# Performance work log

Measured on AMD Instinct MI355X. Metric: run time of the kernel, lower is better.

## Reference

```python
import jax, jax.numpy as jnp
import numpy as np

N, IN_DIM, LAT, NB = 4096, 3000, 64, 2
SINKHORN_ITERS = 3


def _bce_logits(x, y):
    # torch BCEWithLogitsLoss, mean reduction, numerically stable
    return jnp.mean(jnp.maximum(x, 0.0) - x * y + jnp.log1p(jnp.exp(-jnp.abs(x))))


def _forward(feature_set, adj_set, graph_neigh_set, label_CSL_set, dist_mat_set,
             enc_W, dec_W, Ms, disc_W, disc_b, perm_idx):
    nb = feature_set.shape[0]
    hs = []
    loss_sl = 0.0
    loss_feat = 0.0
    for k in range(nb):  # small fixed loop over slices
        x, adj, mask, lab = feature_set[k], adj_set[k], graph_neigh_set[k], label_CSL_set[k]
        h = adj @ (x @ enc_W[k])            # GCN encode: spmm(adj, x @ W)
        out = adj @ (h @ dec_W[k])          # GCN decode
        x_a = x[perm_idx[k]]                # permutation(x): row shuffle
        h_a = adj @ (x_a @ enc_W[k])
        hr, har = jax.nn.relu(h), jax.nn.relu(h_a)

        def readout(emb):
            vsum = mask @ emb
            ge = vsum / mask.sum(1, keepdims=True)
            nrm = jnp.linalg.norm(ge, axis=1, keepdims=True)
            return ge / jnp.maximum(nrm, 1e-12)   # F.normalize p=2

        g = jax.nn.sigmoid(readout(hr))
        g_a = jax.nn.sigmoid(readout(har))

        def disc(c, hp, hm):
            s1 = jnp.einsum('nd,de,ne->n', hp, disc_W, c) + disc_b[0]
            s2 = jnp.einsum('nd,de,ne->n', hm, disc_W, c) + disc_b[0]
            return jnp.stack([s1, s2], axis=1)  # [N,2]

        ret = disc(g, hr, har)
        ret_a = disc(g_a, har, hr)
        loss_sl = loss_sl + _bce_logits(ret, lab) + _bce_logits(ret_a, lab)
        loss_feat = loss_feat + jnp.mean((x - out) ** 2)
        hs.append(h)

    loss_align = 0.0; loss_align_fix = 0.0; loss_maintain = 0.0
    loss_marginal = 0.0; loss_sparsity = 0.0
    for k in range(1, nb):
        src, tgt = hs[k - 1], hs[k]
        M = Ms[k - 1]
        m1, m2 = src.shape[0], tgt.shape[0]
        C = (src @ M) @ (tgt @ M).T / jnp.sqrt(jnp.float32(M.shape[0]))
        P = jax.nn.softmax(C, axis=1) / m1
        # NonSquareSinkhornKnopp.fit: alternate row/col normalization to uniform marginals
        for _ in range(SINKHORN_ITERS):
            P = P / (m1 * P.sum(1, keepdims=True))
            P = P / (m2 * P.sum(0, keepdims=True))
        cxy = P / P.sum(1, keepdims=True)
        cyx = P.T / P.T.sum(1, keepdims=True)
        # cdist(src, tgt)
        d2 = jnp.sum(src ** 2, 1)[:, None] + jnp.sum(tgt ** 2, 1)[None, :] - 2.0 * (src @ tgt.T)
        cd = jnp.sqrt(jnp.maximum(d2, 1e-12))
        loss_align = loss_align + jnp.sum(P * cd)
        f0, f1 = feature_set[k - 1], feature_set[k]
        loss_align_fix = loss_align_fix + jnp.mean((f0 - cxy @ f1) ** 2) + jnp.mean((f1 - cyx @ f0) ** 2)
        D0, D1 = dist_mat_set[k - 1], dist_mat_set[k]
        diff1 = D0 - cxy @ (D1 @ cxy.T)
        diff2 = D1 - cyx @ (D0 @ cyx.T)
        loss_maintain = loss_maintain + jnp.linalg.norm(diff1) / m1 + jnp.linalg.norm(diff2) / m2
        # replicate torch F.kl_div(input, target) = mean(target*(log target - input))
        p = jnp.full((m2,), 1.0 / m2, jnp.float32)
        q = P.sum(0)
        kld_pq = jnp.mean(q * (jnp.log(q) - p))
        kld_pp = jnp.mean(p * (jnp.log(p) - p))
        loss_marginal = loss_marginal + (kld_pq - kld_pp) * m2
        loss_sparsity = loss_sparsity - jnp.sum(P * jnp.log(P + 1e-10))
    return jnp.stack([loss_sl, loss_feat, loss_align, loss_align_fix,
                      loss_maintain, loss_marginal, loss_sparsity])


def setup_inputs():
    key = jax.random.key(0)
    ks = jax.random.split(key, 12)
    feature_set = jax.random.normal(ks[0], (NB, N, IN_DIM), jnp.float32)
    A = jax.random.uniform(ks[1], (NB, N, N), jnp.float32)
    adj_set = A / A.sum(-1, keepdims=True)  # row-stochastic dense stand-in for normalized sparse adj
    mask = (jax.random.uniform(ks[2], (NB, N, N)) < 0.01).astype(jnp.float32)
    graph_neigh_set = mask + jnp.eye(N, dtype=jnp.float32)[None]  # nonzero row sums
    lab = jnp.concatenate([jnp.ones((N, 1)), jnp.zeros((N, 1))], axis=1).astype(jnp.float32)
    label_CSL_set = jnp.broadcast_to(lab, (NB, N, 2))
    D = jax.random.uniform(ks[3], (NB, N, N), jnp.float32)
    dist_mat_set = 0.5 * (D + jnp.swapaxes(D, 1, 2))
    perm_idx = jnp.stack([jax.random.permutation(ks[4 + i], N) for i in range(NB)]).astype(jnp.int32)
    s_enc = np.float32(np.sqrt(2.0 / (IN_DIM + LAT)))
    enc_W = jax.random.normal(ks[6], (NB, IN_DIM, LAT), jnp.float32) * s_enc
    dec_W = jax.random.normal(ks[7], (NB, LAT, IN_DIM), jnp.float32) * s_enc
    s_lat = np.float32(np.sqrt(1.0 / LAT))
    Ms = jax.random.normal(ks[8], (NB - 1, LAT, LAT), jnp.float32) * s_lat
    disc_W = jax.random.normal(ks[9], (LAT, LAT), jnp.float32) * s_lat
    disc_b = jnp.zeros((1,), jnp.float32)
    return dict(feature_set=feature_set, adj_set=adj_set, graph_neigh_set=graph_neigh_set,
                label_CSL_set=label_CSL_set, dist_mat_set=dist_mat_set, perm_idx=perm_idx,
                enc_W=enc_W, dec_W=dec_W, Ms=Ms, disc_W=disc_W, disc_b=disc_b)


def reference(feature_set, adj_set, graph_neigh_set, label_CSL_set, dist_mat_set,
              perm_idx, enc_W, dec_W, Ms, disc_W, disc_b):
    return _forward(feature_set, adj_set, graph_neigh_set, label_CSL_set, dist_mat_set,
                    enc_W, dec_W, Ms, disc_W, disc_b, perm_idx)
```

## Files before the change

kernel.cpp:

```cpp
#include <hip/hip_runtime.h>
#include <cmath>

constexpr int kN   = 4096;
constexpr int kIN  = 3000;
constexpr int kINp = 3072;
constexpr int kLAT = 64;

enum { SL = 0, FEAT, ALN, FXA, FXB, SM1, SM2, SPS, NSLOT };

typedef __bf16 bf16x8 __attribute__((ext_vector_type(8)));
typedef float f32x4 __attribute__((ext_vector_type(4)));
typedef unsigned short u16x8 __attribute__((ext_vector_type(8)));
typedef unsigned short u16x4 __attribute__((ext_vector_type(4)));

template<bool IS_MAX>
__device__ __forceinline__ float blk_red(float v) {
  __shared__ float buf[8];
  #pragma unroll
  for (int s = 32; s > 0; s >>= 1) {
    float o = __shfl_down(v, s, 64);
    v = IS_MAX ? fmaxf(v, o) : (v + o);
  }
  int lane = threadIdx.x & 63, wv = threadIdx.x >> 6, nw = blockDim.x >> 6;
  __syncthreads();
  if (lane == 0) buf[wv] = v;
  __syncthreads();
  float r = buf[0];
  for (int i = 1; i < nw; i++) r = IS_MAX ? fmaxf(r, buf[i]) : (r + buf[i]);
  return r;
}

__device__ __forceinline__ float wave_red_sum(float v) {
  #pragma unroll
  for (int s = 32; s > 0; s >>= 1) v += __shfl_down(v, s, 64);
  return v;
}

__device__ __forceinline__ unsigned short f2bf(float f) {
  unsigned u = __builtin_bit_cast(unsigned, f);
  u += 0x7fffu + ((u >> 16) & 1u);
  return (unsigned short)(u >> 16);
}
__device__ __forceinline__ float bf2f(unsigned short h) {
  return __builtin_bit_cast(float, (unsigned)h << 16);
}

__device__ __forceinline__ void gload16(const unsigned short* g, unsigned short* l) {
  __builtin_amdgcn_global_load_lds(
      (const __attribute__((address_space(1))) unsigned int*)g,
      (__attribute__((address_space(3))) unsigned int*)l, 16, 0, 0);
}

#define VMW(n) asm volatile("s_waitcnt vmcnt(" #n ")" ::: "memory")

__global__ __launch_bounds__(512, 2)
void g8_mfma_k(const unsigned short* __restrict__ A, const unsigned short* __restrict__ Bt,
               unsigned short* __restrict__ Cb, const float* __restrict__ rowdiv, int K)
{
  __shared__ unsigned short AB[65536];

  int orig = blockIdx.x;
  int x = orig & 7, tt = orig >> 3;
  int bx = tt >> 1, by = x * 2 + (tt & 1);
  const int row0 = by * 256, col0 = bx * 256;

  const int t = threadIdx.x, l = t & 63, wv = t >> 6;
  const int wr = wv >> 2, wc = wv & 3;
  const int lr = l & 15;
  const int sA = (l >> 4) ^ ((lr >> 1) & 3);

  f32x4 acc[8][4];
  #pragma unroll
  for (int i = 0; i < 8; i++)
    #pragma unroll
    for (int j = 0; j < 4; j++) acc[i][j] = (f32x4){0.f, 0.f, 0.f, 0.f};

  const int NT = K >> 6;
  const int NI = NT >> 1;

  const int srow  = l >> 2;
  const int sslot = (l & 3) ^ ((l >> 3) & 3);
  const unsigned short* Ap = A  + (size_t)(row0 + srow) * K + sslot * 8;
  const unsigned short* Bp = Bt + (size_t)(col0 + srow) * K + sslot * 8;

  auto STG = [&](int tile, int r) {
    if (tile >= NT) return;
    int buf = tile & 1, ks = r >> 1;
    const unsigned short* src = (r & 1) ? Bp : Ap;
    unsigned short* dst = AB + buf * 32768 + r * 8192;
    size_t koff = (size_t)tile * 64 + ks * 32;
    #pragma unroll
    for (int j = 0; j < 2; j++) {
      int c = wv * 2 + j;
      gload16(src + (size_t)c * 16 * K + koff, dst + c * 512);
    }
  };

  u16x8 af[8], bfv[2];

#define MFMA16(AV, BV, ACC) \
  ACC = __builtin_amdgcn_mfma_f32_16x16x32_bf16( \
      __builtin_bit_cast(bf16x8, AV), __builtin_bit_cast(bf16x8, BV), ACC, 0, 0, 0)

#define PH_A(WN, BUF, KS, STILE, SR)                                           \
  {                                                                            \
    if ((WN) == 8) VMW(8); else if ((WN) == 4) VMW(4);                         \
    else if ((WN) == 0) VMW(0);                                                \
    __builtin_amdgcn_s_barrier();                                              \
    {                                                                          \
      const unsigned short* ab = &AB[(BUF) * 32768 + (KS) * 16384];            \
      _Pragma("unroll")                                                        \
      for (int mi = 0; mi < 8; mi++)                                           \
        af[mi] = *(const u16x8*)&ab[(wr * 128 + mi * 16 + lr) * 32 + sA * 8];  \
      const unsigned short* bb = ab + 8192;                                    \
      bfv[0] = *(const u16x8*)&bb[(wc * 64 +  0 + lr) * 32 + sA * 8];          \
      bfv[1] = *(const u16x8*)&bb[(wc * 64 + 16 + lr) * 32 + sA * 8];          \
    }                                                                          \
    if ((STILE) >= 0) STG(STILE, SR);                                          \
    asm volatile("s_waitcnt lgkmcnt(0)" ::: "memory");                         \
    __builtin_amdgcn_sched_barrier(0);                                         \
    __builtin_amdgcn_s_setprio(1);                                             \
    _Pragma("unroll")                                                          \
    for (int mi = 0; mi < 8; mi++) {                                           \
      MFMA16(af[mi], bfv[0], acc[mi][0]);                                      \
      MFMA16(af[mi], bfv[1], acc[mi][1]);                                      \
    }                                                                          \
    __builtin_amdgcn_s_setprio(0);                                             \
    __builtin_amdgcn_s_barrier();                                              \
  }

#define PH_B(BUF, KS, STILE, SR)                                               \
  {                                                                            \
    __builtin_amdgcn_s_barrier();                                              \
    {                                                                          \
      const unsigned short* bb = &AB[(BUF) * 32768 + (KS) * 16384 + 8192];     \
      bfv[0] = *(const u16x8*)&bb[(wc * 64 + 32 + lr) * 32 + sA * 8];          \
      bfv[1] = *(const u16x8*)&bb[(wc * 64 + 48 + lr) * 32 + sA * 8];          \
    }                                                                          \
    if ((STILE) >= 0) STG(STILE, SR);                                          \
    asm volatile("s_waitcnt lgkmcnt(0)" ::: "memory");                         \
    __builtin_amdgcn_sched_barrier(0);                                         \
    __builtin_amdgcn_s_setprio(1);                                             \
    _Pragma("unroll")                                                          \
    for (int mi = 0; mi < 8; mi++) {                                           \
      MFMA16(af[mi], bfv[0], acc[mi][2]);                                      \
      MFMA16(af[mi], bfv[1], acc[mi][3]);                                      \
    }                                                                          \
    __builtin_amdgcn_s_setprio(0);                                             \
    __builtin_amdgcn_s_barrier();                                              \
  }

  STG(0, 0); STG(0, 1); STG(0, 2); STG(0, 3); STG(1, 0); STG(1, 1);

  for (int i = 0; i < NI - 1; ++i) {
    int T = 2 * i;
    PH_A(8, 0, 0, T + 1, 2);
    PH_B(   0, 0, T + 1, 3);
    PH_A(8, 0, 1, T + 2, 0);
    PH_B(   0, 1, T + 2, 1);
    PH_A(8, 1, 0, T + 2, 2);
    PH_B(   1, 0, T + 2, 3);
    PH_A(8, 1, 1, T + 3, 0);
    PH_B(   1, 1, T + 3, 1);
  }
  {
    int T = 2 * (NI - 1);
    PH_A(8, 0, 0, T + 1, 2);
    PH_B(   0, 0, T + 1, 3);
    PH_A(8, 0, 1, -1, 0);
    PH_B(   0, 1, -1, 0);
    PH_A(4, 1, 0, -1, 0);
    PH_B(   1, 0, -1, 0);
    PH_A(0, 1, 1, -1, 0);
    PH_B(   1, 1, -1, 0);
  }
#undef PH_A
#undef PH_B
#undef MFMA16

  const int lcol = l & 15, lrow = (l >> 4) << 2;
  #pragma unroll
  for (int mi = 0; mi < 8; mi++) {
    int rr = row0 + wr * 128 + mi * 16 + lrow;
    #pragma unroll
    for (int nn = 0; nn < 4; nn++) {
      int cc = col0 + wc * 64 + nn * 16 + lcol;
      #pragma unroll
      for (int r = 0; r < 4; r++) {
        float v = acc[mi][nn][r];
        if (rowdiv) v /= rowdiv[rr + r];
        Cb[(size_t)(rr + r) * 4096 + cc] = f2bf(v);
      }
    }
  }
}

template<int EPI, int XBF>
__global__ __launch_bounds__(256)
void bt_mfma_k(const unsigned short* __restrict__ A, const unsigned short* __restrict__ Bt,
               unsigned short* __restrict__ Cb, float* __restrict__ Cf,
               const void* __restrict__ Xv,
               const float* __restrict__ rowdiv, const float* __restrict__ coldiv,
               float* __restrict__ slot, int gx, int Nc, int K, int ldX, int sym)
{
  __shared__ unsigned short AB[3 * 8192];

  int orig = blockIdx.x;
  int bx, by;
  if (EPI == 2 && sym) {
    int x = orig & 7, i = orig >> 3;
    int u = x * 66 + i;
    float disc = 4225.f - 8.f * (float)u;
    by = (int)((65.f - sqrtf(fmaxf(disc, 0.f))) * 0.5f);
    while (by > 0 && 32 * by - by * (by - 1) / 2 > u) by--;
    while (32 * (by + 1) - (by + 1) * by / 2 <= u) by++;
    bx = by + (u - (32 * by - by * (by - 1) / 2));
  } else {
    int x = orig & 7, tt = orig >> 3;
    bx = tt >> 2;
    by = x * 4 + (tt & 3);
  }
  const int row0 = by * 128, col0 = bx * 128;

  const int t = threadIdx.x, l = t & 63, wv = t >> 6;
  const int wr = wv >> 1, wc = wv & 1;
  const int lr = l & 15, lkh = (l >> 4) << 3;

  f32x4 acc[4][4];
  #pragma unroll
  for (int i = 0; i < 4; i++)
    #pragma unroll
    for (int j = 0; j < 4; j++) acc[i][j] = (f32x4){0.f, 0.f, 0.f, 0.f};

  const int srow = l >> 2;
  const int sk   = (l & 3) << 3;
  const unsigned short* Ab = A  + (size_t)(row0 + srow) * K + sk;
  const unsigned short* Bb = Bt + (size_t)(col0 + srow) * K + sk;

  const int NT = K >> 5;

  auto STAGE = [&](int kt, int buf) {
    unsigned short* As = AB + buf * 8192;
    unsigned short* Bs = As + 4096;
    int k0 = kt << 5;
    #pragma unroll
    for (int h2 = 0; h2 < 2; h2++) {
      int c = wv * 2 + h2;
      gload16(Ab + (size_t)c * 16 * K + k0, As + c * 512);
      gload16(Bb + (size_t)c * 16 * K + k0, Bs + c * 512);
    }
  };

  STAGE(0, 0);
  if (NT > 1) STAGE(1, 1);
  if (NT > 2) STAGE(2, 2);
  int cur = 0;

  for (int kt = 0; kt < NT; ++kt) {
    int ahead = NT - 1 - kt;
    if (ahead >= 2)      { VMW(8); }
    else if (ahead == 1) { VMW(4); }
    else                 { VMW(0); }
    __builtin_amdgcn_sched_barrier(0);
    __builtin_amdgcn_s_barrier();

    const unsigned short* As = AB + cur * 8192;
    const unsigned short* Bs = As + 4096;
    u16x8 af[4], bfv[4];
    #pragma unroll
    for (int mi = 0; mi < 4; mi++)
      af[mi] = *(const u16x8*)&As[(wr * 64 + mi * 16 + lr) * 32 + lkh];
    #pragma unroll
    for (int ni = 0; ni < 4; ni++)
      bfv[ni] = *(const u16x8*)&Bs[(wc * 64 + ni * 16 + lr) * 32 + lkh];
    #pragma unroll
    for (int mi = 0; mi < 4; mi++)
      #pragma unroll
      for (int ni = 0; ni < 4; ni++)
        acc[mi][ni] = __builtin_amdgcn_mfma_f32_16x16x32_bf16(
            __builtin_bit_cast(bf16x8, af[mi]),
            __builtin_bit_cast(bf16x8, bfv[ni]), acc[mi][ni], 0, 0, 0);

    __builtin_amdgcn_s_barrier();
    if (kt + 3 < NT) STAGE(kt + 3, cur);
    cur = (cur == 2) ? 0 : cur + 1;
  }

  const int lcol = l & 15, lrow = (l >> 4) << 2;
  if (EPI == 1) {
    #pragma unroll
    for (int mi = 0; mi < 4; mi++) {
      int rr = row0 + wr * 64 + mi * 16 + lrow;
      #pragma unroll
      for (int ni = 0; ni < 4; ni++) {
        int cc = col0 + wc * 64 + ni * 16 + lcol;
        #pragma unroll
        for (int r = 0; r < 4; r++)
          Cf[(size_t)(rr + r) * 4096 + cc] = acc[mi][ni][r];
      }
    }
  } else if (EPI == 2) {
    const float* Xf = (const float*)Xv;
    const unsigned short* Xh = (const unsigned short*)Xv;
    float part = 0.f;
    #pragma unroll
    for (int mi = 0; mi < 4; mi++) {
      int rr = row0 + wr * 64 + mi * 16 + lrow;
      #pragma unroll
      for (int ni = 0; ni < 4; ni++) {
        int cc = col0 + wc * 64 + ni * 16 + lcol;
        if (cc < Nc) {
          float cd = coldiv ? coldiv[cc] : 1.f;
          #pragma unroll
          for (int r = 0; r < 4; r++) {
            float v = acc[mi][ni][r];
            if (rowdiv) v /= rowdiv[rr + r];
            v /= cd;
            size_t xi = (size_t)(rr + r) * ldX + cc;
            float xval = XBF ? bf2f(Xh[xi]) : Xf[xi];
            float d = xval - v;
            part = fmaf(d, d, part);
          }
        }
      }
    }
    part = blk_red<false>(part);
    if (t == 0) {
      float wgt = (sym && col0 > row0) ? 2.f : 1.f;
      atomicAdd(slot, part * wgt);
    }
  } else {
    const unsigned short* Ph = (const unsigned short*)Xv;
    float a = 0.f, sp = 0.f;
    #pragma unroll
    for (int mi = 0; mi < 4; mi++) {
      int rr = row0 + wr * 64 + mi * 16 + lrow;
      #pragma unroll
      for (int ni = 0; ni < 4; ni++) {
        int cc = col0 + wc * 64 + ni * 16 + lcol;
        #pragma unroll
        for (int r = 0; r < 4; r++) {
          float g = acc[mi][ni][r];
          float p = bf2f(Ph[(size_t)(rr + r) * ldX + cc]);
          float d2 = rowdiv[rr + r] + coldiv[cc] - 2.f * g;
          a = fmaf(p, sqrtf(fmaxf(d2, 1e-12f)), a);
          sp = fmaf(p, logf(p + 1e-10f), sp);
        }
      }
    }
    a = blk_red<false>(a);
    sp = blk_red<false>(sp);
    if (t == 0) { atomicAdd(&slot[ALN], a); atomicAdd(&slot[SPS], sp); }
  }
}

__global__ __launch_bounds__(256)
void ns_mfma_k(const unsigned short* __restrict__ A, const unsigned short* __restrict__ Bt,
               float* __restrict__ C, int Nc, int K, int KC, int ldC)
{
  __shared__ unsigned short AB[2 * 8192];
  int ks = blockIdx.x & 15, strip = blockIdx.x >> 4;
  const int row0 = strip * 128;
  const int kbase = ks * KC;

  const int t = threadIdx.x, l = t & 63, wv = t >> 6;
  const int wr = wv >> 1, wc = wv & 1;
  const int lr = l & 15, lkh = (l >> 4) << 3;

  f32x4 acc[4][4];
  #pragma unroll
  for (int i = 0; i < 4; i++)
    #pragma unroll
    for (int j = 0; j < 4; j++) acc[i][j] = (f32x4){0.f, 0.f, 0.f, 0.f};

  const int srow = l >> 2;
  const int sk   = (l & 3) << 3;
  const unsigned short* Ab = A  + (size_t)(row0 + srow) * K + kbase + sk;
  const unsigned short* Bb = Bt + (size_t)srow * K + kbase + sk;

  const int NT = KC >> 5;

  auto STAGE = [&](int kt, int buf) {
    unsigned short* As = AB + buf * 8192;
    unsigned short* Bs = As + 4096;
    int k0 = kt << 5;
    #pragma unroll
    for (int h2 = 0; h2 < 2; h2++) {
      int c = wv * 2 + h2;
      gload16(Ab + (size_t)c * 16 * K + k0, As + c * 512);
      gload16(Bb + (size_t)c * 16 * K + k0, Bs + c * 512);
    }
  };

  STAGE(0, 0);
  if (NT > 1) STAGE(1, 1);
  int cur = 0;

  for (int kt = 0; kt < NT; ++kt) {
    if (kt + 1 < NT) { VMW(4); }
    else             { VMW(0); }
    __builtin_amdgcn_sched_barrier(0);
    __builtin_amdgcn_s_barrier();

    const unsigned short* As = AB + cur * 8192;
    const unsigned short* Bs = As + 4096;
    u16x8 af[4], bfv[4];
    #pragma unroll
    for (int mi = 0; mi < 4; mi++)
      af[mi] = *(const u16x8*)&As[(wr * 64 + mi * 16 + lr) * 32 + lkh];
    #pragma unroll
    for (int ni = 0; ni < 4; ni++)
      bfv[ni] = *(const u16x8*)&Bs[(wc * 64 + ni * 16 + lr) * 32 + lkh];
    #pragma unroll
    for (int mi = 0; mi < 4; mi++)
      #pragma unroll
      for (int ni = 0; ni < 4; ni++)
        acc[mi][ni] = __builtin_amdgcn_mfma_f32_16x16x32_bf16(
            __builtin_bit_cast(bf16x8, af[mi]),
            __builtin_bit_cast(bf16x8, bfv[ni]), acc[mi][ni], 0, 0, 0);

    __builtin_amdgcn_s_barrier();
    if (kt + 2 < NT) STAGE(kt + 2, cur);
    cur ^= 1;
  }

  const int lcol = l & 15, lrow = (l >> 4) << 2;
  #pragma unroll
  for (int mi = 0; mi < 4; mi++) {
    int rr = row0 + wr * 64 + mi * 16 + lrow;
    #pragma unroll
    for (int ni = 0; ni < 4; ni++) {
      int cc = wc * 64 + ni * 16 + lcol;
      if (cc < Nc) {
        #pragma unroll
        for (int r = 0; r < 4; r++)
          atomicAdd(&C[(size_t)(rr + r) * ldC + cc], acc[mi][ni][r]);
      }
    }
  }
}

__global__ void cvt_k(const float* __restrict__ s, unsigned short* __restrict__ d,
                      int n8, float scale)
{
  int i = blockIdx.x * 256 + threadIdx.x;
  if (i < n8) {
    float4 a = ((const float4*)s)[2 * i], b = ((const float4*)s)[2 * i + 1];
    u16x8 w;
    w[0] = f2bf(a.x * scale); w[1] = f2bf(a.y * scale);
    w[2] = f2bf(a.z * scale); w[3] = f2bf(a.w * scale);
    w[4] = f2bf(b.x * scale); w[5] = f2bf(b.y * scale);
    w[6] = f2bf(b.z * scale); w[7] = f2bf(b.w * scale);
    ((u16x8*)d)[i] = w;
  }
}

__global__ void cvt_rs_k(const float* __restrict__ s, unsigned short* __restrict__ d,
                         float* __restrict__ mrs)
{
  int i = blockIdx.x * 256 + threadIdx.x;
  float4 a = ((const float4*)s)[2 * i], b = ((const float4*)s)[2 * i + 1];
  u16x8 w;
  w[0] = f2bf(a.x); w[1] = f2bf(a.y); w[2] = f2bf(a.z); w[3] = f2bf(a.w);
  w[4] = f2bf(b.x); w[5] = f2bf(b.y); w[6] = f2bf(b.z); w[7] = f2bf(b.w);
  ((u16x8*)d)[i] = w;
  float s8 = a.x + a.y + a.z + a.w + b.x + b.y + b.z + b.w;
  float ws = wave_red_sum(s8);
  if ((threadIdx.x & 63) == 0) atomicAdd(&mrs[i >> 9], ws);
}

__global__ void cvt_pad_k(const float* __restrict__ s, unsigned short* __restrict__ d)
{
  int i = blockIdx.x * 256 + threadIdx.x;
  int row = i / 384, c8 = (i - row * 384) * 8;
  u16x8 w = (u16x8)0;
  if (c8 < kIN) {
    const float* sp = s + (size_t)row * kIN + c8;
    float4 a = *(const float4*)sp, b = *(const float4*)(sp + 4);
    w[0] = f2bf(a.x); w[1] = f2bf(a.y); w[2] = f2bf(a.z); w[3] = f2bf(a.w);
    w[4] = f2bf(b.x); w[5] = f2bf(b.y); w[6] = f2bf(b.z); w[7] = f2bf(b.w);
  }
  ((u16x8*)d)[i] = w;
}

__global__ void cvt_cols_k(const float* __restrict__ s, unsigned short* __restrict__ d)
{
  int i = blockIdx.x * 256 + threadIdx.x;
  int row = i >> 3, c8 = (i & 7) * 8;
  const float* sp = s + (size_t)row * 128 + c8;
  float4 a = *(const float4*)sp, b = *(const float4*)(sp + 4);
  u16x8 w;
  w[0] = f2bf(a.x); w[1] = f2bf(a.y); w[2] = f2bf(a.z); w[3] = f2bf(a.w);
  w[4] = f2bf(b.x); w[5] = f2bf(b.y); w[6] = f2bf(b.z); w[7] = f2bf(b.w);
  ((u16x8*)d)[i] = w;
}

template<bool RELU>
__global__ void tr_k(const float* __restrict__ src, unsigned short* __restrict__ dst,
                     int R, int C, int sld, int dld)
{
  __shared__ float tile[32][33];
  int c0 = blockIdx.x * 32, r0 = blockIdx.y * 32;
  int tr_ = threadIdx.x >> 3, tc4 = (threadIdx.x & 7) << 2;
  #pragma unroll
  for (int j = 0; j < 4; j++) {
    int r = r0 + tr_, c = c0 + tc4 + j;
    float v = (r < R && c < C) ? src[(size_t)r * sld + c] : 0.f;
    if (RELU) v = fmaxf(v, 0.f);
    tile[tr_][tc4 + j] = v;
  }
  __syncthreads();
  u16x4 wv;
  #pragma unroll
  for (int j = 0; j < 4; j++) wv[j] = f2bf(tile[tc4 + j][tr_]);
  *(u16x4*)&dst[(size_t)(c0 + tr_) * dld + r0 + tc4] = wv;
}

__global__ __launch_bounds__(256)
void gemm_small_k(const float* __restrict__ A, const float* __restrict__ B,
                  float* __restrict__ C, int M, int Nc, int K,
                  int ldA, int ldB, int ldC)
{
  __shared__ float As[16][68];
  __shared__ float Bs[16][68];
  int tid = threadIdx.x;
  int tx = tid & 15, ty = tid >> 4;
  int row0 = blockIdx.y * 64, col0 = blockIdx.x * 64;
  float acc[4][4] = {};

  for (int k0 = 0; k0 < K; k0 += 16) {
    {
      int m = tid >> 2, kk = (tid & 3) << 2;
      const float* ap = A + (size_t)(row0 + m) * ldA + k0 + kk;
      float4 v = *(const float4*)ap;
      As[kk + 0][m] = v.x; As[kk + 1][m] = v.y; As[kk + 2][m] = v.z; As[kk + 3][m] = v.w;
    }
    {
      int kk = tid >> 4, c = (tid & 15) << 2;
      const float* bp = B + (size_t)(k0 + kk) * ldB + col0 + c;
      #pragma unroll
      for (int i = 0; i < 4; i++)
        Bs[kk][c + i] = (col0 + c + i < Nc) ? bp[i] : 0.f;
    }
    __syncthreads();
    #pragma unroll
    for (int kk = 0; kk < 16; kk++) {
      float4 a4 = *(const float4*)&As[kk][ty << 2];
      float4 b4 = *(const float4*)&Bs[kk][tx << 2];
      float av[4] = {a4.x, a4.y, a4.z, a4.w};
      float bv[4] = {b4.x, b4.y, b4.z, b4.w};
      #pragma unroll
      for (int i = 0; i < 4; i++)
        #pragma unroll
        for (int j = 0; j < 4; j++)
          acc[i][j] = fmaf(av[i], bv[j], acc[i][j]);
    }
    __syncthreads();
  }
  #pragma unroll
  for (int i = 0; i < 4; i++) {
    int r = row0 + (ty << 2) + i;
    #pragma unroll
    for (int j = 0; j < 4; j++) {
      int c = col0 + (tx << 2) + j;
      if (c < Nc) C[(size_t)r * ldC + c] = acc[i][j];
    }
  }
}

__global__ __launch_bounds__(256)
void sink_k(float* __restrict__ P, unsigned short* __restrict__ Pb,
            const float* __restrict__ cs_in, float* __restrict__ cs_out,
            float* __restrict__ rs, int mode)
{
  int tid = threadIdx.x;
  int r0 = blockIdx.x * 8;
  float csl[16] = {};
  float cdiv[16];
  if (mode != 0) {
    #pragma unroll
    for (int t = 0; t < 4; t++) {
      float4 c4 = ((const float4*)cs_in)[tid + t * 256];
      cdiv[4 * t + 0] = 1.f / (4096.f * c4.x);
      cdiv[4 * t + 1] = 1.f / (4096.f * c4.y);
      cdiv[4 * t + 2] = 1.f / (4096.f * c4.z);
      cdiv[4 * t + 3] = 1.f / (4096.f * c4.w);
    }
  }
  for (int rr = 0; rr < 8; rr++) {
    int row = r0 + rr;
    float4* prow = (float4*)(P + (size_t)row * 4096);
    float4 r[4];
    #pragma unroll
    for (int t = 0; t < 4; t++) r[t] = prow[tid + t * 256];

    if (mode == 0) {
      float m = -3.4e38f;
      #pragma unroll
      for (int t = 0; t < 4; t++)
        m = fmaxf(m, fmaxf(fmaxf(r[t].x, r[t].y), fmaxf(r[t].z, r[t].w)));
      m = blk_red<true>(m);
      float s = 0.f;
      #pragma unroll
      for (int t = 0; t < 4; t++) {
        r[t].x = expf(r[t].x - m); r[t].y = expf(r[t].y - m);
        r[t].z = expf(r[t].z - m); r[t].w = expf(r[t].w - m);
        s += r[t].x + r[t].y + r[t].z + r[t].w;
      }
      s = blk_red<false>(s);
      float f = 1.f / (s * 4096.f);
      #pragma unroll
      for (int t = 0; t < 4; t++) {
        r[t].x *= f; r[t].y *= f; r[t].z *= f; r[t].w *= f;
        prow[tid + t * 256] = r[t];
        csl[4 * t + 0] += r[t].x; csl[4 * t + 1] += r[t].y;
        csl[4 * t + 2] += r[t].z; csl[4 * t + 3] += r[t].w;
      }
    } else {
      float s = 0.f;
      #pragma unroll
      for (int t = 0; t < 4; t++) {
        r[t].x *= cdiv[4 * t + 0]; r[t].y *= cdiv[4 * t + 1];
        r[t].z *= cdiv[4 * t + 2]; r[t].w *= cdiv[4 * t + 3];
        s += r[t].x + r[t].y + r[t].z + r[t].w;
      }
      s = blk_red<false>(s);
      if (mode == 1) {
        float f = 1.f / (4096.f * s);
        #pragma unroll
        for (int t = 0; t < 4; t++) {
          r[t].x *= f; r[t].y *= f; r[t].z *= f; r[t].w *= f;
          prow[tid + t * 256] = r[t];
          csl[4 * t + 0] += r[t].x; csl[4 * t + 1] += r[t].y;
          csl[4 * t + 2] += r[t].z; csl[4 * t + 3] += r[t].w;
        }
      } else {
        if (tid == 0) rs[row] = s;
        #pragma unroll
        for (int t = 0; t < 4; t++) {
          prow[tid + t * 256] = r[t];
          u16x4 w;
          w[0] = f2bf(r[t].x); w[1] = f2bf(r[t].y);
          w[2] = f2bf(r[t].z); w[3] = f2bf(r[t].w);
          *(u16x4*)&Pb[(size_t)row * 4096 + 4 * (tid + t * 256)] = w;
          csl[4 * t + 0] += r[t].x; csl[4 * t + 1] += r[t].y;
          csl[4 * t + 2] += r[t].z; csl[4 * t + 3] += r[t].w;
        }
      }
    }
  }
  #pragma unroll
  for (int t = 0; t < 4; t++) {
    int j = 4 * (tid + t * 256);
    atomicAdd(&cs_out[j + 0], csl[4 * t + 0]);
    atomicAdd(&cs_out[j + 1], csl[4 * t + 1]);
    atomicAdd(&cs_out[j + 2], csl[4 * t + 2]);
    atomicAdd(&cs_out[j + 3], csl[4 * t + 3]);
  }
}

__global__ void relu_k(const float* __restrict__ in, float* __restrict__ out, int n)
{
  int i = blockIdx.x * blockDim.x + threadIdx.x;
  if (i < n) out[i] = fmaxf(in[i], 0.f);
}

__global__ void gather_k(float* __restrict__ XP, const int* __restrict__ perm)
{
  int gid = blockIdx.x * 256 + threadIdx.x;
  int i = gid >> 6, j = gid & 63;
  XP[(size_t)i * 128 + 64 + j] = XP[(size_t)perm[i] * 128 + j];
}

__global__ void sqnorm_k(const float* __restrict__ H, int ld, float* __restrict__ outv)
{
  int gid = blockIdx.x * 256 + threadIdx.x;
  int row = gid >> 6, j = gid & 63;
  float v = H[(size_t)row * ld + j];
  float p = wave_red_sum(v * v);
  if (j == 0) outv[row] = p;
}

__global__ void readout_k(const float* __restrict__ vs2, const float* __restrict__ mrs,
                          float* __restrict__ g2)
{
  int q = blockIdx.x, j = threadIdx.x;
  float v = vs2[(size_t)q * 64 + j] / mrs[q >> 1];
  float p = v * v;
  #pragma unroll
  for (int s = 1; s < 64; s <<= 1) p += __shfl_xor(p, s, 64);
  float nrm = sqrtf(p);
  v = v / fmaxf(nrm, 1e-12f);
  g2[(size_t)q * 64 + j] = 1.f / (1.f + expf(-v));
}

__device__ __forceinline__ float bce_term(float x, float y) {
  return fmaxf(x, 0.f) - x * y + log1pf(expf(-fabsf(x)));
}

__global__ void disc_k(const float* __restrict__ G2, const float* __restrict__ W2,
                       const float* __restrict__ lab, const float* __restrict__ bptr,
                       float* __restrict__ acc)
{
  int i = blockIdx.x, j = threadIdx.x;
  float gj  = G2[(size_t)(2 * i) * 64 + j];
  float gaj = G2[(size_t)(2 * i + 1) * 64 + j];
  float hw  = W2[(size_t)(2 * i) * 64 + j];
  float haw = W2[(size_t)(2 * i + 1) * 64 + j];
  float s1 = hw * gj, s2 = haw * gj, s1a = haw * gaj, s2a = hw * gaj;
  #pragma unroll
  for (int s = 1; s < 64; s <<= 1) {
    s1  += __shfl_xor(s1, s, 64);
    s2  += __shfl_xor(s2, s, 64);
    s1a += __shfl_xor(s1a, s, 64);
    s2a += __shfl_xor(s2a, s, 64);
  }
  if (j == 0) {
    float b = bptr[0];
    float y0 = lab[i * 2 + 0], y1 = lab[i * 2 + 1];
    float t = bce_term(s1 + b, y0) + bce_term(s2 + b, y1)
            + bce_term(s1a + b, y0) + bce_term(s2a + b, y1);
    atomicAdd(&acc[SL], t);
  }
}

__global__ __launch_bounds__(256)
void finalize_k(const float* __restrict__ acc, const float* __restrict__ cs,
                float* __restrict__ out)
{
  int tid = threadIdx.x;
  float invm2 = 1.f / (float)kN;
  float t = 0.f;
  for (int j = tid; j < kN; j += 256) {
    float q = cs[j];
    t += q * (logf(q) - invm2);
  }
  t = blk_red<false>(t);
  if (tid == 0) {
    float kld_pq = t * invm2;
    float kld_pp = invm2 * (logf(invm2) - invm2);
    out[0] = acc[SL] / (2.f * (float)kN);
    out[1] = acc[FEAT] / ((float)kN * (float)kIN);
    out[2] = acc[ALN];
    out[3] = (acc[FXA] + acc[FXB]) / ((float)kN * (float)kIN);
    out[4] = sqrtf(acc[SM1]) / (float)kN + sqrtf(acc[SM2]) / (float)kN;
    out[5] = (kld_pq - kld_pp) * (float)kN;
    out[6] = -acc[SPS];
  }
}

extern "C" void kernel_launch(void* const* d_in, const int* in_sizes, int n_in,
                              void* d_out, int out_size, void* d_ws, size_t ws_size,
                              hipStream_t stream)
{
  (void)in_sizes; (void)n_in; (void)out_size; (void)ws_size;
  const float* feat  = (const float*)d_in[0];
  const float* adjs  = (const float*)d_in[1];
  const float* gmask = (const float*)d_in[2];
  const float* labs  = (const float*)d_in[3];
  const float* dists = (const float*)d_in[4];
  const int*   perms = (const int*)d_in[5];
  const float* encW  = (const float*)d_in[6];
  const float* decW  = (const float*)d_in[7];
  const float* MsW   = (const float*)d_in[8];
  const float* discW = (const float*)d_in[9];
  const float* discb = (const float*)d_in[10];
  float* out = (float*)d_out;

  const size_t SZNN = (size_t)kN * kN;

  char* cur = (char*)d_ws;
  auto alloc = [&](size_t bytes) {
    char* p = cur;
    cur += (bytes + 255) & ~(size_t)255;
    return p;
  };
  float* P            = (float*)alloc(SZNN * 4);
  unsigned short* Pb  = (unsigned short*)alloc(SZNN * 2);
  unsigned short* PbT = (unsigned short*)alloc(SZNN * 2);
  unsigned short* Db  = (unsigned short*)alloc(SZNN * 2);
  unsigned short* ajb = (unsigned short*)alloc(SZNN * 2);
  unsigned short* xb  = (unsigned short*)alloc((size_t)kN * kINp * 2);
  unsigned short* dWtb= (unsigned short*)alloc((size_t)kINp * kLAT * 2);
  unsigned short* ahb = (unsigned short*)alloc((size_t)kN * kLAT * 2);
  unsigned short* encWtp = (unsigned short*)alloc((size_t)128 * kINp * 2);
  unsigned short* XPt = (unsigned short*)alloc((size_t)128 * kN * 2);
  unsigned short* hbTp= (unsigned short*)alloc((size_t)128 * kN * 2);
  unsigned short* HRt = (unsigned short*)alloc((size_t)128 * kN * 2);
  unsigned short* smb = (unsigned short*)alloc((size_t)kN * kLAT * 2);
  unsigned short* tmb = (unsigned short*)alloc((size_t)kN * kLAT * 2);
  unsigned short* h0b = (unsigned short*)alloc((size_t)kN * kLAT * 2);
  unsigned short* h1b = (unsigned short*)alloc((size_t)kN * kLAT * 2);
  float* XP  = (float*)alloc((size_t)kN * 128 * 4);
  float* HH0 = (float*)alloc((size_t)kN * 128 * 4);
  float* HH1 = (float*)alloc((size_t)kN * 128 * 4);
  float* HR  = (float*)alloc((size_t)kN * 128 * 4);
  float* VS  = (float*)alloc((size_t)kN * 128 * 4);
  float* G2  = (float*)alloc((size_t)kN * 128 * 4);
  float* W2  = (float*)alloc((size_t)kN * 128 * 4);
  float* SM_ = (float*)alloc((size_t)kN * kLAT * 4);
  float* TM_ = (float*)alloc((size_t)kN * kLAT * 4);
  float* ah  = (float*)alloc((size_t)kN * kLAT * 4);
  float* sns = (float*)alloc(kN * 4);
  float* snt = (float*)alloc(kN * 4);
  float* rs  = (float*)alloc(kN * 4);
  float* cs  = (float*)alloc(kN * 4);
  float* csA = (float*)alloc(kN * 4);
  float* csB = (float*)alloc(kN * 4);
  float* mrs = (float*)alloc(kN * 4);
  float* acc = (float*)alloc(NSLOT * 4);

  unsigned short* Tb  = (unsigned short*)P;
  unsigned short* ftb = ajb;

  hipMemsetAsync(acc, 0, NSLOT * sizeof(float), stream);

  for (int k = 0; k < 2; k++) {
    const float* x    = feat  + (size_t)k * kN * kIN;
    const float* adj  = adjs  + (size_t)k * SZNN;
    const float* msk  = gmask + (size_t)k * SZNN;
    const float* lab  = labs  + (size_t)k * kN * 2;
    const int*   perm = perms + (size_t)k * kN;
    const float* eW   = encW  + (size_t)k * kIN * kLAT;
    const float* dW   = decW  + (size_t)k * kLAT * kIN;
    float* HHk = (k == 0) ? HH0 : HH1;

    cvt_pad_k<<<6144, 256, 0, stream>>>(x, xb);
    hipMemsetAsync(encWtp, 0, (size_t)128 * kINp * 2, stream);
    tr_k<false><<<dim3(2, (kIN + 31) / 32), 256, 0, stream>>>(eW, encWtp, kIN, kLAT, kLAT, kINp);
    hipMemsetAsync(XP, 0, (size_t)kN * 128 * 4, stream);
    ns_mfma_k<<<512, 256, 0, stream>>>(xb, encWtp, XP, kLAT, kINp, kINp / 16, 128);
    gather_k<<<kN * 64 / 256, 256, 0, stream>>>(XP, perm);
    tr_k<false><<<dim3(4, 128), 256, 0, stream>>>(XP, XPt, kN, 128, 128, kN);
    cvt_k<<<(int)(SZNN / 8 / 256), 256, 0, stream>>>(adj, ajb, (int)(SZNN / 8), 1.f);
    hipMemsetAsync(HHk, 0, (size_t)kN * 128 * 4, stream);
    ns_mfma_k<<<512, 256, 0, stream>>>(ajb, XPt, HHk, 128, kN, kN / 16, 128);
    hipMemsetAsync(hbTp, 0, (size_t)128 * kN * 2, stream);
    tr_k<false><<<dim3(2, 128), 256, 0, stream>>>(HHk, hbTp, kN, kLAT, 128, kN);
    hipMemsetAsync(ah, 0, (size_t)kN * kLAT * 4, stream);
    ns_mfma_k<<<512, 256, 0, stream>>>(ajb, hbTp, ah, kLAT, kN, kN / 16, kLAT);
    cvt_k<<<128, 256, 0, stream>>>(ah, ahb, kN * kLAT / 8, 1.f);
    tr_k<false><<<dim3(kINp / 32, 2), 256, 0, stream>>>(dW, dWtb, kLAT, kIN, kIN, kLAT);
    bt_mfma_k<2, 1><<<(kINp / 128) * 32, 256, 0, stream>>>(
        ahb, dWtb, nullptr, nullptr, xb, nullptr, nullptr, &acc[FEAT],
        kINp / 128, kIN, kLAT, kINp, 0);
    relu_k<<<kN * 128 / 256, 256, 0, stream>>>(HHk, HR, kN * 128);
    tr_k<true><<<dim3(4, 128), 256, 0, stream>>>(HHk, HRt, kN, 128, 128, kN);
    hipMemsetAsync(mrs, 0, kN * 4, stream);
    cvt_rs_k<<<(int)(SZNN / 8 / 256), 256, 0, stream>>>(msk, ajb, mrs);
    hipMemsetAsync(VS, 0, (size_t)kN * 128 * 4, stream);
    ns_mfma_k<<<512, 256, 0, stream>>>(ajb, HRt, VS, 128, kN, kN / 16, 128);
    readout_k<<<2 * kN, 64, 0, stream>>>(VS, mrs, G2);
    gemm_small_k<<<dim3(1, 128), 256, 0, stream>>>(HR, discW, W2, 2 * kN, kLAT, kLAT,
                                                   kLAT, kLAT, kLAT);
    disc_k<<<kN, 64, 0, stream>>>(G2, W2, lab, discb, acc);
  }

  const float* f0 = feat;
  const float* f1 = feat + (size_t)kN * kIN;
  const float* D0 = dists;
  const float* D1 = dists + SZNN;

  gemm_small_k<<<dim3(1, 64), 256, 0, stream>>>(HH0, MsW, SM_, kN, kLAT, kLAT, 128, kLAT, kLAT);
  gemm_small_k<<<dim3(1, 64), 256, 0, stream>>>(HH1, MsW, TM_, kN, kLAT, kLAT, 128, kLAT, kLAT);
  cvt_k<<<128, 256, 0, stream>>>(SM_, smb, kN * kLAT / 8, 0.125f);
  cvt_k<<<128, 256, 0, stream>>>(TM_, tmb, kN * kLAT / 8, 1.f);
  bt_mfma_k<1, 0><<<1024, 256, 0, stream>>>(smb, tmb, nullptr, P, nullptr, nullptr, nullptr,
                                            nullptr, 32, kN, kLAT, 0, 0);

  hipMemsetAsync(csA, 0, kN * 4, stream);
  sink_k<<<512, 256, 0, stream>>>(P, nullptr, nullptr, csA, nullptr, 0);
  hipMemsetAsync(csB, 0, kN * 4, stream);
  sink_k<<<512, 256, 0, stream>>>(P, nullptr, csA, csB, nullptr, 1);
  hipMemsetAsync(csA, 0, kN * 4, stream);
  sink_k<<<512, 256, 0, stream>>>(P, nullptr, csB, csA, nullptr, 1);
  hipMemsetAsync(cs, 0, kN * 4, stream);
  sink_k<<<512, 256, 0, stream>>>(P, Pb, csA, cs, rs, 2);

  tr_k<false><<<dim3(kN / 32, kN / 32), 256, 0, stream>>>(P, PbT, kN, kN, kN, kN);

  cvt_cols_k<<<128, 256, 0, stream>>>(HH0, h0b);
  cvt_cols_k<<<128, 256, 0, stream>>>(HH1, h1b);
  sqnorm_k<<<kN * 64 / 256, 256, 0, stream>>>(HH0, 128, sns);
  sqnorm_k<<<kN * 64 / 256, 256, 0, stream>>>(HH1, 128, snt);
  bt_mfma_k<3, 1><<<1024, 256, 0, stream>>>(h0b, h1b, nullptr, nullptr, Pb, sns, snt, acc,
                                            32, kN, kLAT, kN, 0);

  tr_k<false><<<dim3(kINp / 32, kN / 32), 256, 0, stream>>>(f1, ftb, kN, kIN, kIN, kN);
  bt_mfma_k<2, 0><<<(kINp / 128) * 32, 256, 0, stream>>>(
      Pb, ftb, nullptr, nullptr, f0, rs, nullptr, &acc[FXA], kINp / 128, kIN, kN, kIN, 0);
  tr_k<false><<<dim3(kINp / 32, kN / 32), 256, 0, stream>>>(f0, ftb, kN, kIN, kIN, kN);
  bt_mfma_k<2, 0><<<(kINp / 128) * 32, 256, 0, stream>>>(
      PbT, ftb, nullptr, nullptr, f1, cs, nullptr, &acc[FXB], kINp / 128, kIN, kN, kIN, 0);

  cvt_k<<<(int)(SZNN / 8 / 256), 256, 0, stream>>>(D1, Db, (int)(SZNN / 8), 1.f);
  g8_mfma_k<<<256, 512, 0, stream>>>(Pb, Db, Tb, rs, kN);
  bt_mfma_k<2, 0><<<528, 256, 0, stream>>>(Tb, Pb, nullptr, nullptr, D0, nullptr, rs,
                                           &acc[SM1], 32, kN, kN, kN, 1);
  cvt_k<<<(int)(SZNN / 8 / 256), 256, 0, stream>>>(D0, Db, (int)(SZNN / 8), 1.f);
  g8_mfma_k<<<256, 512, 0, stream>>>(PbT, Db, Tb, cs, kN);
  bt_mfma_k<2, 0><<<528, 256, 0, stream>>>(Tb, PbT, nullptr, nullptr, D1, nullptr, cs,
                                           &acc[SM2], 32, kN, kN, kN, 1);

  finalize_k<<<1, 256, 0, stream>>>(acc, cs, out);
}
```

Measured before the change: 2.061 ms.

## Restructure GEMM phase barriers/waitcnt placement and stage epilogue through LDS

Merges the two phase macros into one and moves the vmcnt wait and barrier to the end of each phase. This lets LDS reads for the next phase start before the barrier, so global-to-LDS loads overlap better with MFMA work. The epilogue now stages bf16 results through LDS per wave and writes 8-byte vectors to global memory, replacing scattered 2-byte stores. The risk is a race, because LDS reads now happen right after a barrier that no longer waits on the loads, and the epilogue reuses the AB buffer.

```diff
diff --git a/kernel.cpp b/kernel.cpp
--- a/kernel.cpp
+++ b/kernel.cpp
@@ -102,95 +102,93 @@
   ACC = __builtin_amdgcn_mfma_f32_16x16x32_bf16( \
       __builtin_bit_cast(bf16x8, AV), __builtin_bit_cast(bf16x8, BV), ACC, 0, 0, 0)
 
-#define PH_A(WN, BUF, KS, STILE, SR)                                           \
+#define PH(ISA, VN, BUF, KS, STILE, SR)                                        \
   {                                                                            \
-    if ((WN) == 8) VMW(8); else if ((WN) == 4) VMW(4);                         \
-    else if ((WN) == 0) VMW(0);                                                \
-    __builtin_amdgcn_s_barrier();                                              \
     {                                                                          \
       const unsigned short* ab = &AB[(BUF) * 32768 + (KS) * 16384];            \
-      _Pragma("unroll")                                                        \
-      for (int mi = 0; mi < 8; mi++)                                           \
-        af[mi] = *(const u16x8*)&ab[(wr * 128 + mi * 16 + lr) * 32 + sA * 8];  \
       const unsigned short* bb = ab + 8192;                                    \
-      bfv[0] = *(const u16x8*)&bb[(wc * 64 +  0 + lr) * 32 + sA * 8];          \
-      bfv[1] = *(const u16x8*)&bb[(wc * 64 + 16 + lr) * 32 + sA * 8];          \
+      if (ISA) {                                                               \
+        _Pragma("unroll")                                                      \
+        for (int mi = 0; mi < 8; mi++)                                         \
+          af[mi] = *(const u16x8*)&ab[(wr * 128 + mi * 16 + lr) * 32 + sA * 8];\
+        bfv[0] = *(const u16x8*)&bb[(wc * 64 +  0 + lr) * 32 + sA * 8];        \
+        bfv[1] = *(const u16x8*)&bb[(wc * 64 + 16 + lr) * 32 + sA * 8];        \
+      } else {                                                                 \
+        bfv[0] = *(const u16x8*)&bb[(wc * 64 + 32 + lr) * 32 + sA * 8];        \
+        bfv[1] = *(const u16x8*)&bb[(wc * 64 + 48 + lr) * 32 + sA * 8];        \
+      }                                                                        \
     }                                                                          \
     if ((STILE) >= 0) STG(STILE, SR);                                          \
+    __builtin_amdgcn_sched_barrier(0);                                         \
+    __builtin_amdgcn_s_barrier();                                              \
     asm volatile("s_waitcnt lgkmcnt(0)" ::: "memory");                         \
     __builtin_amdgcn_sched_barrier(0);                                         \
     __builtin_amdgcn_s_setprio(1);                                             \
     _Pragma("unroll")                                                          \
     for (int mi = 0; mi < 8; mi++) {                                           \
-      MFMA16(af[mi], bfv[0], acc[mi][0]);                                      \
-      MFMA16(af[mi], bfv[1], acc[mi][1]);                                      \
+      MFMA16(af[mi], bfv[0], acc[mi][(ISA) ? 0 : 2]);                          \
+      MFMA16(af[mi], bfv[1], acc[mi][(ISA) ? 1 : 3]);                          \
     }                                                                          \
     __builtin_amdgcn_s_setprio(0);                                             \
+    if ((VN) == 8) VMW(8); else if ((VN) == 4) VMW(4);                         \
+    else if ((VN) == 0) VMW(0);                                                \
+    __builtin_amdgcn_sched_barrier(0);                                         \
     __builtin_amdgcn_s_barrier();                                              \
   }
 
-#define PH_B(BUF, KS, STILE, SR)                                               \
-  {                                                                            \
-    __builtin_amdgcn_s_barrier();                                              \
-    {                                                                          \
-      const unsigned short* bb = &AB[(BUF) * 32768 + (KS) * 16384 + 8192];     \
-      bfv[0] = *(const u16x8*)&bb[(wc * 64 + 32 + lr) * 32 + sA * 8];          \
-      bfv[1] = *(const u16x8*)&bb[(wc * 64 + 48 + lr) * 32 + sA * 8];          \
-    }                                                                          \
-    if ((STILE) >= 0) STG(STILE, SR);                                          \
-    asm volatile("s_waitcnt lgkmcnt(0)" ::: "memory");                         \
-    __builtin_amdgcn_sched_barrier(0);                                         \
-    __builtin_amdgcn_s_setprio(1);                                             \
-    _Pragma("unroll")                                                          \
-    for (int mi = 0; mi < 8; mi++) {                                           \
-      MFMA16(af[mi], bfv[0], acc[mi][2]);                                      \
-      MFMA16(af[mi], bfv[1], acc[mi][3]);                                      \
-    }                                                                          \
-    __builtin_amdgcn_s_setprio(0);                                             \
-    __builtin_amdgcn_s_barrier();                                              \
-  }
-
   STG(0, 0); STG(0, 1); STG(0, 2); STG(0, 3); STG(1, 0); STG(1, 1);
+  VMW(8);
+  __builtin_amdgcn_sched_barrier(0);
+  __builtin_amdgcn_s_barrier();
 
   for (int i = 0; i < NI - 1; ++i) {
     int T = 2 * i;
-    PH_A(8, 0, 0, T + 1, 2);
-    PH_B(   0, 0, T + 1, 3);
-    PH_A(8, 0, 1, T + 2, 0);
-    PH_B(   0, 1, T + 2, 1);
-    PH_A(8, 1, 0, T + 2, 2);
-    PH_B(   1, 0, T + 2, 3);
-    PH_A(8, 1, 1, T + 3, 0);
-    PH_B(   1, 1, T + 3, 1);
+    PH(1, -1, 0, 0, T + 1, 2);
+    PH(0,  8, 0, 0, T + 1, 3);
+    PH(1, -1, 0, 1, T + 2, 0);
+    PH(0,  8, 0, 1, T + 2, 1);
+    PH(1, -1, 1, 0, T + 2, 2);
+    PH(0,  8, 1, 0, T + 2, 3);
+    PH(1, -1, 1, 1, T + 3, 0);
+    PH(0,  8, 1, 1, T + 3, 1);
   }
   {
     int T = 2 * (NI - 1);
-    PH_A(8, 0, 0, T + 1, 2);
-    PH_B(   0, 0, T + 1, 3);
-    PH_A(8, 0, 1, -1, 0);
-    PH_B(   0, 1, -1, 0);
-    PH_A(4, 1, 0, -1, 0);
-    PH_B(   1, 0, -1, 0);
-    PH_A(0, 1, 1, -1, 0);
-    PH_B(   1, 1, -1, 0);
-  }
-#undef PH_A
-#undef PH_B
+    PH(1, -1, 0, 0, T + 1, 2);
+    PH(0,  8, 0, 0, T + 1, 3);
+    PH(1, -1, 0, 1, -1, 0);
+    PH(0,  4, 0, 1, -1, 0);
+    PH(1, -1, 1, 0, -1, 0);
+    PH(0,  0, 1, 0, -1, 0);
+    PH(1, -1, 1, 1, -1, 0);
+    PH(0, -1, 1, 1, -1, 0);
+  }
+#undef PH
 #undef MFMA16
 
-  const int lcol = l & 15, lrow = (l >> 4) << 2;
-  #pragma unroll
-  for (int mi = 0; mi < 8; mi++) {
-    int rr = row0 + wr * 128 + mi * 16 + lrow;
-    #pragma unroll
-    for (int nn = 0; nn < 4; nn++) {
-      int cc = col0 + wc * 64 + nn * 16 + lcol;
-      #pragma unroll
-      for (int r = 0; r < 4; r++) {
-        float v = acc[mi][nn][r];
-        if (rowdiv) v /= rowdiv[rr + r];
-        Cb[(size_t)(rr + r) * 4096 + cc] = f2bf(v);
-      }
+  unsigned short* lw = AB + wv * 8192;
+  const int lcol = l & 15, lrow4 = l >> 4;
+  #pragma unroll
+  for (int half = 0; half < 2; ++half) {
+    #pragma unroll
+    for (int mi2 = 0; mi2 < 4; ++mi2) {
+      int mi = half * 4 + mi2;
+      #pragma unroll
+      for (int nn = 0; nn < 4; ++nn)
+        #pragma unroll
+        for (int r = 0; r < 4; ++r) {
+          float v = acc[mi][nn][r];
+          if (rowdiv) v /= rowdiv[row0 + wr * 128 + mi * 16 + lrow4 * 4 + r];
+          lw[(mi2 * 16 + lrow4 * 4 + r) * 68 + nn * 16 + lcol] = f2bf(v);
+        }
+    }
+    #pragma unroll
+    for (int rr2 = 0; rr2 < 16; ++rr2) {
+      int lrr = rr2 * 4 + lrow4;
+      u16x4 w4 = *(const u16x4*)&lw[lrr * 68 + lcol * 4];
+      int grow = row0 + wr * 128 + half * 64 + lrr;
+      int gcol = col0 + wc * 64 + lcol * 4;
+      *(u16x4*)&Cb[(size_t)grow * 4096 + gcol] = w4;
     }
   }
 }
```

After: 2.051 ms. No clear change (-0.5%).
